# Kernel tuning notes

Measured on AMD Instinct MI355X. Metric: run time of the kernel, lower is better.

The kernel has to match this reference:

```python
import jax, jax.numpy as jnp
import numpy as np

NSEG = 65  # instance ids live in [0, NSEG); must match setup_inputs fill_max
EPS = 1e-8


def setup_inputs() -> dict:
    key = jax.random.key(0)
    k1, k2 = jax.random.split(key)
    B, C, H, W = 8, 4, 1024, 1024
    logit = jax.random.normal(k1, (B, C, H, W), dtype=jnp.float32)
    inst_gt = jax.random.randint(k2, (B, H, W), 0, NSEG, dtype=jnp.int32)
    return {"logit": logit, "inst_gt": inst_gt}


def reference(logit, inst_gt):
    B, C, H, W = logit.shape
    N = H * W
    # softmax over channel dim (as F.softmax(logit, dim=1))
    p = jax.nn.softmax(logit, axis=1)                      # [B, C, H, W]
    p = p.reshape(B, C, N).transpose(0, 2, 1).reshape(B * N, C)  # [B*N, C]
    # one fused segment reduce over all batches: offset ids per batch element
    seg = (inst_gt.reshape(B, N) + jnp.arange(B, dtype=inst_gt.dtype)[:, None] * NSEG).reshape(-1)
    sums = jax.ops.segment_sum(p, seg, num_segments=B * NSEG)        # [B*NSEG, C]
    sumsq = jax.ops.segment_sum(p * p, seg, num_segments=B * NSEG)   # [B*NSEG, C]
    cnt = jax.ops.segment_sum(jnp.ones((B * N,), p.dtype), seg, num_segments=B * NSEG)  # [B*NSEG]
    cnt = cnt[:, None]                                               # [B*NSEG, 1]
    # unbiased variance per (batch, instance, channel): (sumsq - sum^2/n) / (n-1)
    n_safe = jnp.where(cnt > 0, cnt, 1.0)
    denom = jnp.where(cnt > 1, cnt - 1.0, 1.0)
    var = (sumsq - sums * sums / n_safe) / denom                     # [B*NSEG, C]
    var = var.reshape(B, NSEG, C)
    cnt = cnt.reshape(B, NSEG, 1)
    nonzero_id = (jnp.arange(NSEG) != 0)[None, :, None]              # skip background id 0
    # only instances with more than 1 pixel contribute variance
    valid = nonzero_id & (cnt > 1.0)
    sum_var = jnp.sum(jnp.where(valid, var, 0.0), axis=(1, 2))       # [B]
    # len(inst_ids): number of distinct nonzero ids present in each image
    num_ids = jnp.sum(jnp.where(nonzero_id[..., 0] & (cnt[..., 0] > 0.0), 1.0, 0.0), axis=1)  # [B]
    loss = jnp.mean(sum_var / (num_ids + EPS))
    return loss
```

## Files before the change

kernel.cpp:

```cpp
#include <hip/hip_runtime.h>


typedef unsigned short u16x2 __attribute__((ext_vector_type(2)));
typedef unsigned int   u32x4 __attribute__((ext_vector_type(4)));
typedef short          s16x8 __attribute__((ext_vector_type(8)));
typedef float          f32x4 __attribute__((ext_vector_type(4)));

constexpr int   B_    = 8;
constexpr int   SEGS  = 64;
constexpr int   VALS  = 5;
constexpr float EPS_  = 1e-8f;

constexpr int PLANE   = 528;
constexpr int NSLOT   = 9;
constexpr int BUFSZ   = NSLOT * PLANE;
constexpr int WLDS    = 2 * BUFSZ;
constexpr int LDS_SZ  = (4 * WLDS > 16384) ? 4 * WLDS : 16384;

__device__ __forceinline__ unsigned asu(float f)  { return __float_as_uint(f); }
__device__ __forceinline__ float    asf(unsigned u){ return __uint_as_float(u); }

__global__ __launch_bounds__(256, 4) void vl_accum(const float* __restrict__ logit,
                                                   const int*   __restrict__ inst,
                                                   float* __restrict__ accOut,
                                                   int N, int ppb)
{
    __shared__ __align__(16) unsigned char lds[LDS_SZ];

    const int tid  = threadIdx.x;
    const int wid  = tid >> 6;
    const int lane = tid & 63;
    const int col  = lane & 15;
    const int quad = lane >> 4;
    const int wbase = wid * WLDS;

    const bool selLds = (col < 4) | (col >= 8 && col < 12);
    const unsigned cword = (col == 4) ? 0x3F803F80u : 0u;
    const int pl = (col < 4) ? (2 * col)
                 : ((col >= 8 && col < 12) ? (2 * (col - 8) + 1) : 0);
    const int bRd0   = wbase + pl * PLANE + quad * 16;
    const int segRd0 = wbase + 8 * PLANE + quad * 16;
    const int segWr0 = wbase + 8 * PLANE + lane * 8;

    u16x2 rowdup[4];
#pragma unroll
    for (int t = 0; t < 4; ++t) {
        unsigned short rw = (unsigned short)(t * 16 + col);
        rowdup[t] = (u16x2){rw, rw};
    }
    const u16x2 one2  = (u16x2){1, 1};
    const u16x2 negb  = (u16x2){0xC080, 0xC080};
    const u16x2 posb  = (u16x2){0x3F80, 0x3F80};

    const int b = blockIdx.y;
    const float* __restrict__ l0 = logit + (size_t)b * 4 * N;
    const int*   __restrict__ ib = inst  + (size_t)b * N;

    f32x4 acc0a = {0,0,0,0}, acc1a = {0,0,0,0}, acc2a = {0,0,0,0}, acc3a = {0,0,0,0};
    f32x4 acc0b = {0,0,0,0}, acc1b = {0,0,0,0}, acc2b = {0,0,0,0}, acc3b = {0,0,0,0};

    const int blockStart = blockIdx.x * ppb;
    const int rounds = ppb >> 10;
    const int base0  = blockStart + (wid << 8) + (lane << 2);

#define LOAD_ROUND(R, X0, X1, X2, X3, SG)                                       \
    {                                                                           \
        const int q  = base0 + ((R) << 10);                                     \
        const bool ok = (q + 4 <= N);                                           \
        const int qc = ok ? q : 0;                                              \
        X0 = *(const float4*)(l0 + qc);                                         \
        X1 = *(const float4*)(l0 + (size_t)N     + qc);                         \
        X2 = *(const float4*)(l0 + (size_t)2 * N + qc);                         \
        X3 = *(const float4*)(l0 + (size_t)3 * N + qc);                         \
        int4 sgt = *(const int4*)(ib + qc);                                     \
        SG = ok ? sgt : make_int4(0, 0, 0, 0);                                  \
    }

#define SOFTMAX4(X0, X1, X2, X3, P0, P1, P2, QQ)                                \
    {                                                                           \
        const float sc0[4] = {X0.x, X0.y, X0.z, X0.w};                          \
        const float sc1[4] = {X1.x, X1.y, X1.z, X1.w};                          \
        const float sc2[4] = {X2.x, X2.y, X2.z, X2.w};                          \
        const float sc3[4] = {X3.x, X3.y, X3.z, X3.w};                          \
        _Pragma("unroll")                                                       \
        for (int i = 0; i < 4; ++i) {                                           \
            float va = sc0[i], vb = sc1[i], vc = sc2[i], vd = sc3[i];           \
            float m  = fmaxf(fmaxf(va, vb), fmaxf(vc, vd));                     \
            float e0 = __expf(va - m);                                          \
            float e1 = __expf(vb - m);                                          \
            float e2 = __expf(vc - m);                                          \
            float e3 = __expf(vd - m);                                          \
            float rr = 1.0f / (e0 + e1 + e2 + e3);                              \
            float q0 = e0 * rr, q1 = e1 * rr, q2 = e2 * rr, q3 = e3 * rr;       \
            P0[i] = q0; P1[i] = q1; P2[i] = q2;                                 \
            QQ[i] = q0*q0 + q1*q1 + q2*q2 + q3*q3;                              \
        }                                                                       \
    }

#define STAGE_PLANE(BOFF, P, ARR)                                               \
    {                                                                           \
        unsigned a0 = asu(ARR[0]), a1 = asu(ARR[1]);                            \
        unsigned a2 = asu(ARR[2]), a3 = asu(ARR[3]);                            \
        unsigned h1m = a1 & 0xFFFF0000u, h3m = a3 & 0xFFFF0000u;                \
        unsigned hi01 = (a0 >> 16) | h1m;                                       \
        unsigned hi23 = (a2 >> 16) | h3m;                                       \
        float l0f = ARR[0] - asf(a0 & 0xFFFF0000u);                             \
        float l1f = ARR[1] - asf(h1m);                                          \
        float l2f = ARR[2] - asf(a2 & 0xFFFF0000u);                             \
        float l3f = ARR[3] - asf(h3m);                                          \
        unsigned lo01 = (asu(l0f) >> 16) | (asu(l1f) & 0xFFFF0000u);            \
        unsigned lo23 = (asu(l2f) >> 16) | (asu(l3f) & 0xFFFF0000u);            \
        *(uint2*)(lds + (BOFF) + wbase + (2*(P)) * PLANE + lane * 8)   = make_uint2(hi01, hi23); \
        *(uint2*)(lds + (BOFF) + wbase + (2*(P)+1) * PLANE + lane * 8) = make_uint2(lo01, lo23); \
    }

#define STAGE_ALL(BOFF, P0, P1, P2, QQ, SG)                                     \
    {                                                                           \
        STAGE_PLANE(BOFF, 0, P0)                                                \
        STAGE_PLANE(BOFF, 1, P1)                                                \
        STAGE_PLANE(BOFF, 2, P2)                                                \
        STAGE_PLANE(BOFF, 3, QQ)                                                \
        unsigned r0 = (unsigned)(SG.x - 1) & 0xFFFFu;                           \
        unsigned r1 = (unsigned)(SG.y - 1) & 0xFFFFu;                           \
        unsigned r2 = (unsigned)(SG.z - 1) & 0xFFFFu;                           \
        unsigned r3 = (unsigned)(SG.w - 1) & 0xFFFFu;                           \
        *(uint2*)(lds + (BOFF) + segWr0) = make_uint2(r0 | (r1 << 16), r2 | (r3 << 16)); \
    }

    if (rounds > 0) {
        float4 cx0, cx1, cx2, cx3; int4 csg;
        LOAD_ROUND(0, cx0, cx1, cx2, cx3, csg)
        float P0[4], P1[4], P2[4], QQ[4];
        SOFTMAX4(cx0, cx1, cx2, cx3, P0, P1, P2, QQ)
        STAGE_ALL(0, P0, P1, P2, QQ, csg)
    }

    for (int r = 0; r < rounds; ++r) {
        float4 nx0, nx1, nx2, nx3; int4 nsg;
        const bool hasNext = (r + 1 < rounds);
        if (hasNext) LOAD_ROUND(r + 1, nx0, nx1, nx2, nx3, nsg)
        __builtin_amdgcn_sched_barrier(0);

        const int bufOff = (r & 1) * BUFSZ;
#pragma unroll
        for (int kt = 0; kt < 8; ++kt) {
            s16x8 braw = *(const s16x8*)(lds + bufOff + bRd0   + kt * 64);
            u32x4 sv   = *(const u32x4*)(lds + bufOff + segRd0 + kt * 64);
            u32x4 bw   = __builtin_bit_cast(u32x4, braw);
#pragma unroll
            for (int i = 0; i < 4; ++i) bw[i] = selLds ? bw[i] : cword;
            s16x8 bfrag = __builtin_bit_cast(s16x8, bw);

#define DO_TILE(T, ACC)                                                         \
            {                                                                   \
                u32x4 fr;                                                       \
                _Pragma("unroll")                                               \
                for (int i = 0; i < 4; ++i) {                                   \
                    u16x2 sp  = __builtin_bit_cast(u16x2, sv[i]);               \
                    u16x2 d   = sp - rowdup[T];                                 \
                    u16x2 mn  = __builtin_elementwise_min(d, one2);             \
                    u16x2 f   = mn * negb + posb;              \
                    fr[i] = __builtin_bit_cast(unsigned, f);                    \
                }                                                               \
                s16x8 afrag = __builtin_bit_cast(s16x8, fr);                    \
                ACC = __builtin_amdgcn_mfma_f32_16x16x32_bf16(afrag, bfrag, ACC, 0, 0, 0); \
            }
            if ((kt & 1) == 0) {
                DO_TILE(0, acc0a) DO_TILE(1, acc1a) DO_TILE(2, acc2a) DO_TILE(3, acc3a)
            } else {
                DO_TILE(0, acc0b) DO_TILE(1, acc1b) DO_TILE(2, acc2b) DO_TILE(3, acc3b)
            }
#undef DO_TILE
        }

        if (hasNext) {
            float P0[4], P1[4], P2[4], QQ[4];
            SOFTMAX4(nx0, nx1, nx2, nx3, P0, P1, P2, QQ)
            const int nOff = ((r + 1) & 1) * BUFSZ;
            STAGE_ALL(nOff, P0, P1, P2, QQ, nsg)
        }
    }
#undef LOAD_ROUND
#undef SOFTMAX4
#undef STAGE_PLANE
#undef STAGE_ALL

    f32x4 acc0 = acc0a + acc0b;
    f32x4 acc1 = acc1a + acc1b;
    f32x4 acc2 = acc2a + acc2b;
    f32x4 acc3 = acc3a + acc3b;

    __syncthreads();
    float* cl = (float*)lds;
    {
        const int base = ((wid * 4) * 64 + lane) * 4;
        *(f32x4*)(cl + base)            = acc0;
        *(f32x4*)(cl + base + 64 * 4)   = acc1;
        *(f32x4*)(cl + base + 128 * 4)  = acc2;
        *(f32x4*)(cl + base + 192 * 4)  = acc3;
    }
    __syncthreads();

    for (int i = tid; i < SEGS * VALS; i += 256) {
        const int row = i / VALS;
        const int cc  = i - row * VALS;
        const int t   = row >> 4;
        const int rr  = row & 15;
        const int g   = rr >> 2;
        const int reg = rr & 3;
        const int lhi = g * 16 + cc;
        const int llo = lhi + 8;
        float v = 0.0f;
#pragma unroll
        for (int w = 0; w < 4; ++w) {
            v += cl[((w * 4 + t) * 64 + lhi) * 4 + reg];
            v += cl[((w * 4 + t) * 64 + llo) * 4 + reg];
        }
        unsafeAtomicAdd(accOut + ((size_t)blockIdx.y * SEGS + row) * VALS + cc, v);
    }
}

__global__ __launch_bounds__(256) void vl_finalize(const float* __restrict__ acc,
                                                   float* __restrict__ out)
{
    __shared__ float sum_var[B_];
    __shared__ float num_ids[B_];
    if (threadIdx.x < B_) { sum_var[threadIdx.x] = 0.0f; num_ids[threadIdx.x] = 0.0f; }
    __syncthreads();

    for (int i = threadIdx.x; i < B_ * SEGS; i += 256) {
        const float* a = acc + (size_t)i * VALS;
        const int b = i >> 6;
        const float cnt = a[4];
        if (cnt > 1.0f) {
            const float inv_n = 1.0f / cnt;
            const float denom = cnt - 1.0f;
            const float s0 = a[0], s1 = a[1], s2 = a[2];
            const float s3 = cnt - s0 - s1 - s2;
            const float ssum2 = s0*s0 + s1*s1 + s2*s2 + s3*s3;
            const float sv = (a[3] - ssum2 * inv_n) / denom;
            atomicAdd(&sum_var[b], sv);
        }
        if (cnt > 0.0f) atomicAdd(&num_ids[b], 1.0f);
    }
    __syncthreads();

    if (threadIdx.x == 0) {
        float loss = 0.0f;
#pragma unroll
        for (int b = 0; b < B_; ++b) loss += sum_var[b] / (num_ids[b] + EPS_);
        out[0] = loss / (float)B_;
    }
}

extern "C" void kernel_launch(void* const* d_in, const int* in_sizes, int n_in,
                              void* d_out, int out_size, void* d_ws, size_t ws_size,
                              hipStream_t stream) {
    const float* logit = (const float*)d_in[0];
    const int*   inst  = (const int*)d_in[1];
    float* out = (float*)d_out;
    float* acc = (float*)d_ws;

    const int totalPix = in_sizes[1];
    const int N = totalPix / B_;

    hipMemsetAsync(acc, 0, (size_t)B_ * SEGS * VALS * sizeof(float), stream);

    const int gridx = 128;
    int ppb = (N + gridx - 1) / gridx;
    ppb = (ppb + 1023) & ~1023;

    dim3 grid(gridx, B_);
    vl_accum<<<grid, 256, 0, stream>>>(logit, inst, acc, N, ppb);
    vl_finalize<<<1, 256, 0, stream>>>(acc, out);
}
```

Before: 219.3 us.

## Software-pipeline LDS reads with inline asm and merge dual accumulators

```diff
diff --git a/kernel.cpp b/kernel.cpp
--- a/kernel.cpp
+++ b/kernel.cpp
@@ -19,6 +19,18 @@
 
 __device__ __forceinline__ unsigned asu(float f)  { return __float_as_uint(f); }
 __device__ __forceinline__ float    asf(unsigned u){ return __uint_as_float(u); }
+
+#define ISSUE_Q(BA, SA, BB, SB, OA, OB)                                         \
+    asm volatile("ds_read_b128 %0, %4 offset:" #OA "\n\t"                       \
+                 "ds_read_b128 %1, %5 offset:" #OA "\n\t"                       \
+                 "ds_read_b128 %2, %4 offset:" #OB "\n\t"                       \
+                 "ds_read_b128 %3, %5 offset:" #OB                              \
+                 : "=&v"(BA), "=&v"(SA), "=&v"(BB), "=&v"(SB)                   \
+                 : "v"(addrB), "v"(addrS));
+
+#define WAITQ(N)                                                                \
+    asm volatile("s_waitcnt lgkmcnt(" #N ")" ::: "memory");                     \
+    __builtin_amdgcn_sched_barrier(0);
 
 __global__ __launch_bounds__(256, 4) void vl_accum(const float* __restrict__ logit,
                                                    const int*   __restrict__ inst,
@@ -56,8 +68,7 @@
     const float* __restrict__ l0 = logit + (size_t)b * 4 * N;
     const int*   __restrict__ ib = inst  + (size_t)b * N;
 
-    f32x4 acc0a = {0,0,0,0}, acc1a = {0,0,0,0}, acc2a = {0,0,0,0}, acc3a = {0,0,0,0};
-    f32x4 acc0b = {0,0,0,0}, acc1b = {0,0,0,0}, acc2b = {0,0,0,0}, acc3b = {0,0,0,0};
+    f32x4 acc0 = {0,0,0,0}, acc1 = {0,0,0,0}, acc2 = {0,0,0,0}, acc3 = {0,0,0,0};
 
     const int blockStart = blockIdx.x * ppb;
     const int rounds = ppb >> 10;
@@ -127,6 +138,31 @@
         *(uint2*)(lds + (BOFF) + segWr0) = make_uint2(r0 | (r1 << 16), r2 | (r3 << 16)); \
     }
 
+#define COMPUTE_KT(BQ, SQ)                                                      \
+    {                                                                           \
+        u32x4 bw = BQ;                                                          \
+        _Pragma("unroll")                                                       \
+        for (int i = 0; i < 4; ++i) bw[i] = selLds ? bw[i] : cword;             \
+        s16x8 bfrag = __builtin_bit_cast(s16x8, bw);                            \
+        u32x4 sv = SQ;                                                          \
+        DO_TILE(0, acc0) DO_TILE(1, acc1) DO_TILE(2, acc2) DO_TILE(3, acc3)     \
+    }
+
+#define DO_TILE(T, ACC)                                                         \
+        {                                                                       \
+            u32x4 fr;                                                           \
+            _Pragma("unroll")                                                   \
+            for (int i = 0; i < 4; ++i) {                                       \
+                u16x2 sp  = __builtin_bit_cast(u16x2, sv[i]);                   \
+                u16x2 d   = sp - rowdup[T];                                     \
+                u16x2 mn  = __builtin_elementwise_min(d, one2);                 \
+                u16x2 f   = mn * negb + posb;                  \
+                fr[i] = __builtin_bit_cast(unsigned, f);                        \
+            }                                                                   \
+            s16x8 afrag = __builtin_bit_cast(s16x8, fr);                        \
+            ACC = __builtin_amdgcn_mfma_f32_16x16x32_bf16(afrag, bfrag, ACC, 0, 0, 0); \
+        }
+
     if (rounds > 0) {
         float4 cx0, cx1, cx2, cx3; int4 csg;
         LOAD_ROUND(0, cx0, cx1, cx2, cx3, csg)
@@ -142,36 +178,26 @@
         __builtin_amdgcn_sched_barrier(0);
 
         const int bufOff = (r & 1) * BUFSZ;
-#pragma unroll
-        for (int kt = 0; kt < 8; ++kt) {
-            s16x8 braw = *(const s16x8*)(lds + bufOff + bRd0   + kt * 64);
-            u32x4 sv   = *(const u32x4*)(lds + bufOff + segRd0 + kt * 64);
-            u32x4 bw   = __builtin_bit_cast(u32x4, braw);
-#pragma unroll
-            for (int i = 0; i < 4; ++i) bw[i] = selLds ? bw[i] : cword;
-            s16x8 bfrag = __builtin_bit_cast(s16x8, bw);
-
-#define DO_TILE(T, ACC)                                                         \
-            {                                                                   \
-                u32x4 fr;                                                       \
-                _Pragma("unroll")                                               \
-                for (int i = 0; i < 4; ++i) {                                   \
-                    u16x2 sp  = __builtin_bit_cast(u16x2, sv[i]);               \
-                    u16x2 d   = sp - rowdup[T];                                 \
-                    u16x2 mn  = __builtin_elementwise_min(d, one2);             \
-                    u16x2 f   = mn * negb + posb;              \
-                    fr[i] = __builtin_bit_cast(unsigned, f);                    \
-                }                                                               \
-                s16x8 afrag = __builtin_bit_cast(s16x8, fr);                    \
-                ACC = __builtin_amdgcn_mfma_f32_16x16x32_bf16(afrag, bfrag, ACC, 0, 0, 0); \
-            }
-            if ((kt & 1) == 0) {
-                DO_TILE(0, acc0a) DO_TILE(1, acc1a) DO_TILE(2, acc2a) DO_TILE(3, acc3a)
-            } else {
-                DO_TILE(0, acc0b) DO_TILE(1, acc1b) DO_TILE(2, acc2b) DO_TILE(3, acc3b)
-            }
-#undef DO_TILE
-        }
+        const unsigned addrB = (unsigned)(unsigned long long)(const void*)(lds + bufOff + bRd0);
+        const unsigned addrS = (unsigned)(unsigned long long)(const void*)(lds + bufOff + segRd0);
+
+        u32x4 b0, s0, b1, s1, b2, s2, b3, s3, b4, s4, b5, s5, b6, s6, b7, s7;
+        ISSUE_Q(b0, s0, b1, s1, 0,   64)
+        ISSUE_Q(b2, s2, b3, s3, 128, 192)
+        WAITQ(4)
+        COMPUTE_KT(b0, s0)
+        COMPUTE_KT(b1, s1)
+        ISSUE_Q(b4, s4, b5, s5, 256, 320)
+        WAITQ(4)
+        COMPUTE_KT(b2, s2)
+        COMPUTE_KT(b3, s3)
+        ISSUE_Q(b6, s6, b7, s7, 384, 448)
+        WAITQ(4)
+        COMPUTE_KT(b4, s4)
+        COMPUTE_KT(b5, s5)
+        WAITQ(0)
+        COMPUTE_KT(b6, s6)
+        COMPUTE_KT(b7, s7)
 
         if (hasNext) {
             float P0[4], P1[4], P2[4], QQ[4];
@@ -180,15 +206,12 @@
             STAGE_ALL(nOff, P0, P1, P2, QQ, nsg)
         }
     }
+#undef DO_TILE
+#undef COMPUTE_KT
 #undef LOAD_ROUND
 #undef SOFTMAX4
 #undef STAGE_PLANE
 #undef STAGE_ALL
-
-    f32x4 acc0 = acc0a + acc0b;
-    f32x4 acc1 = acc1a + acc1b;
-    f32x4 acc2 = acc2a + acc2b;
-    f32x4 acc3 = acc3a + acc3b;
 
     __syncthreads();
     float* cl = (float*)lds;
```

Result: no change. 219.4 us (+0.0%).
